# Optimization experiments

Measured on AMD Instinct MI355X. Metric: run time of the kernel, lower is better.

The kernel has to match this reference:

```python
import jax, jax.numpy as jnp
import numpy as np

INPUT_H = 512
INPUT_W = 512
POOL = 5
BN_EPS = 1e-5


def setup_inputs() -> dict:
    key = jax.random.key(0)
    ks = jax.random.split(key, 8)
    B = 16
    c3 = jax.random.normal(ks[0], (B, 512, 64, 64), jnp.float32)
    c4 = jax.random.normal(ks[1], (B, 1024, 32, 32), jnp.float32)
    xy = jax.random.uniform(ks[2], (B, 10, 4), jnp.float32) * 512.0
    # ensure x1<=x2, y1<=y2 like real detector boxes
    boxes = jnp.concatenate([jnp.minimum(xy[..., :2], xy[..., 2:]),
                             jnp.maximum(xy[..., :2], xy[..., 2:])], axis=-1)
    w_conv = jax.random.normal(ks[3], (512, 1536), jnp.float32) * 0.02  # 1x1 conv kernel
    b_conv = jnp.zeros((512,), jnp.float32)
    bn_gamma = jnp.ones((512,), jnp.float32)
    bn_beta = jnp.zeros((512,), jnp.float32)
    bn_mean = jax.random.normal(ks[4], (512,), jnp.float32) * 0.1
    bn_var = jax.random.uniform(ks[5], (512,), jnp.float32) * 0.5 + 0.5
    return {"c3": c3, "c4": c4, "boxes": boxes, "w_conv": w_conv, "b_conv": b_conv,
            "bn_gamma": bn_gamma, "bn_beta": bn_beta, "bn_mean": bn_mean, "bn_var": bn_var}


def _bin_weights(lo, hi, size, nout):
    """Adaptive-avg-pool bin weights over axis of length `size` for crop [lo,hi).
    Returns [nout, size] row-stochastic matrix (same math as AdaptiveAvgPool1d bins)."""
    length = hi - lo
    k = jnp.arange(nout)
    starts = lo + (k * length) // nout                      # floor(k*L/n)
    ends = lo + ((k + 1) * length + nout - 1) // nout        # ceil((k+1)*L/n)
    idx = jnp.arange(size)
    mask = (idx[None, :] >= starts[:, None]) & (idx[None, :] < ends[:, None])
    return mask.astype(jnp.float32) / (ends - starts)[:, None].astype(jnp.float32)


def reference(c3, c4, boxes, w_conv, b_conv, bn_gamma, bn_beta, bn_mean, bn_var):
    B = c3.shape[0]
    c4u = jax.image.resize(c4, (B, c4.shape[1], c4.shape[2] * 2, c4.shape[3] * 2),
                           method='bilinear')
    fused = jnp.concatenate([c3, c4u], axis=1)               # [B,1536,H,W]
    y = jnp.einsum('bchw,oc->bohw', fused, w_conv) + b_conv[None, :, None, None]
    inv = bn_gamma / jnp.sqrt(bn_var + BN_EPS)               # eval-mode BN
    y = y * inv[None, :, None, None] + (bn_beta - bn_mean * inv)[None, :, None, None]
    attr_blob = jax.nn.relu(y)                               # [B,512,H,W]
    H, W = attr_blob.shape[-2:]
    sx = W / INPUT_W
    sy = H / INPUT_H

    def pool_one(feat, box):  # feat [C,H,W], box [4] -> [C,5,5]
        x1 = jnp.clip(jnp.floor(box[0] * sx), 0, W - 1).astype(jnp.int32)
        y1 = jnp.clip(jnp.floor(box[1] * sy), 0, H - 1).astype(jnp.int32)
        x2 = jnp.clip(jnp.ceil(box[2] * sx), 0, W - 1).astype(jnp.int32)
        y2 = jnp.clip(jnp.ceil(box[3] * sy), 0, H - 1).astype(jnp.int32)
        x2 = jnp.where(x2 <= x1, jnp.minimum(x1 + 1, W), x2)
        y2 = jnp.where(y2 <= y1, jnp.minimum(y1 + 1, H), y2)
        wy = _bin_weights(y1, y2, H, POOL)                   # [5,H]
        wx = _bin_weights(x1, x2, W, POOL)                   # [5,W]
        return jnp.einsum('ph,chw,qw->cpq', wy, feat, wx)

    obj_blob = jax.vmap(lambda f, bx: jax.vmap(lambda b: pool_one(f, b))(bx))(attr_blob, boxes)
    return boxes, obj_blob  # ([B,10,4], [B,10,512,5,5])
```

## Files before the change

### kernel.cpp

```cpp
#include <hip/hip_runtime.h>
#include <stdint.h>

#define FH 64
#define FW 64
#define CIN 1536
#define C3C 512
#define C4C 1024
#define COUT 512
#define BATCH 16
#define NPIX 4096
#define NBOX 10
#define MPAD 256
#define NT 24

typedef float v4f __attribute__((ext_vector_type(4)));

#define GLOAD_LDS16(g, l) __builtin_amdgcn_global_load_lds( \
    (const __attribute__((address_space(1))) void*)(g),     \
    (__attribute__((address_space(3))) void*)(l), 16, 0, 0)

#define BARRIER() asm volatile("s_barrier" ::: "memory")

__device__ __forceinline__ uint32_t pack4_fp8(float a, float b, float c, float d) {
    int lo = __builtin_amdgcn_cvt_pk_fp8_f32(a, b, 0, false);
    int v  = __builtin_amdgcn_cvt_pk_fp8_f32(c, d, lo, true);
    return (uint32_t)v;
}
__device__ __forceinline__ unsigned char f32_to_fp8(float a) {
    return (unsigned char)(__builtin_amdgcn_cvt_pk_fp8_f32(a, a, 0, false) & 0xff);
}

__global__ void prep_bn(const float* __restrict__ bng, const float* __restrict__ bnb,
                        const float* __restrict__ bnm, const float* __restrict__ bnv,
                        const float* __restrict__ bconv,
                        float* __restrict__ scale, float* __restrict__ shift) {
    int o = threadIdx.x;
    if (o < COUT) {
        float inv = bng[o] / sqrtf(bnv[o] + 1e-5f);
        scale[o] = inv * 0.0625f;
        shift[o] = bnb[o] + inv * (bconv[o] - bnm[o]);
    }
}

__global__ void conv_w(const float* __restrict__ w, uint32_t* __restrict__ w8, int n4) {
    int i = blockIdx.x * 256 + threadIdx.x;
    if (i < n4) {
        float4 f = *(const float4*)(w + i * 4);
        w8[i] = pack4_fp8(f.x * 16.0f, f.y * 16.0f, f.z * 16.0f, f.w * 16.0f);
    }
}

__global__ __launch_bounds__(256) void build_fusedT(const float* __restrict__ c3,
                                                    const float* __restrict__ c4,
                                                    unsigned char* __restrict__ fusedT) {
    __shared__ uint32_t lds[64 * 36];
    int ct = blockIdx.x;
    int y  = blockIdx.y;
    int b  = blockIdx.z;
    int t  = threadIdx.x;
    int pg = t & 15;
    int cq = t >> 4;

    #pragma unroll
    for (int r = 0; r < 2; ++r) {
        int cquad = cq + 16 * r;
        float vv[4][4];
        if (ct < 4) {
            int ch = ct * 128 + 4 * cquad;
            const float* src = c3 + (((size_t)(b * C3C + ch) * FH + y) * FW) + 4 * pg;
            #pragma unroll
            for (int k = 0; k < 4; ++k) {
                float4 f = *(const float4*)(src + (size_t)k * (FH * FW));
                vv[k][0] = f.x; vv[k][1] = f.y; vv[k][2] = f.z; vv[k][3] = f.w;
            }
        } else {
            int ch = ct * 128 - 512 + 4 * cquad;
            int jy = y >> 1;
            int jyB = min(max(jy + ((y & 1) ? 1 : -1), 0), 31);
            const float* base = c4 + (size_t)(b * C4C + ch) * 1024;
            #pragma unroll
            for (int k = 0; k < 4; ++k) {
                const float* pc = base + (size_t)k * 1024;
                float2 f0 = *(const float2*)(pc + jy * 32 + 2 * pg);
                float2 f1 = *(const float2*)(pc + jyB * 32 + 2 * pg);
                float rbA = 0.75f * f0.x + 0.25f * f1.x;
                float rbB = 0.75f * f0.y + 0.25f * f1.y;
                float rbm = __shfl_up(rbB, 1, 16);
                float rbp = __shfl_down(rbA, 1, 16);
                if (pg == 0)  rbm = rbA;
                if (pg == 15) rbp = rbB;
                vv[k][0] = 0.75f * rbA + 0.25f * rbm;
                vv[k][1] = 0.75f * rbA + 0.25f * rbB;
                vv[k][2] = 0.75f * rbB + 0.25f * rbA;
                vv[k][3] = 0.75f * rbB + 0.25f * rbp;
            }
        }
        #pragma unroll
        for (int i = 0; i < 4; ++i) {
            int px = 4 * pg + i;
            lds[px * 36 + 4 * ((cquad >> 2) ^ ((px >> 1) & 7)) + (cquad & 3)] =
                pack4_fp8(vv[0][i], vv[1][i], vv[2][i], vv[3][i]);
        }
    }
    __syncthreads();
    int g = t & 7;
    #pragma unroll
    for (int rr = 0; rr < 2; ++rr) {
        int px = (t >> 3) + 32 * rr;
        uint4 w = *(const uint4*)(&lds[px * 36 + 4 * (g ^ ((px >> 1) & 7))]);
        *(uint4*)(fusedT + ((size_t)b * NPIX + y * FW + px) * CIN + ct * 128 + g * 16) = w;
    }
}

__global__ __launch_bounds__(512, 2) void gemm_bn_relu(
        const unsigned char* __restrict__ w8,
        const unsigned char* __restrict__ fusedT,
        const float* __restrict__ scale, const float* __restrict__ shift,
        unsigned char* __restrict__ attr) {
    __shared__ __align__(16) unsigned char lds_a[2][16384];
    __shared__ __align__(16) unsigned char lds_b[2][16384];
    const int t  = threadIdx.x;
    const int n0 = blockIdx.x * 256;
    const int o0 = blockIdx.y * 256;
    const int b  = blockIdx.z;
    const int wave = t >> 6, lane = t & 63;
    const int wm = wave & 1, wn = wave >> 1;
    const int quad = lane >> 4, l16 = lane & 15;
    const int q2 = quad >> 1, q1 = (quad & 1) * 8;
    const int keyq = (l16 >> 1) & 3;
    const int cs0 = ((q2 ^ keyq) * 16) + q1;
    const int cs1 = (((2 + q2) ^ keyq) * 16) + q1;
    const unsigned char* fb = fusedT + (size_t)b * NPIX * CIN;

    const int lrow = t >> 2;
    const int cg   = (t & 3) ^ ((t >> 3) & 3);
    const size_t gA0 = (size_t)(o0 + ((t >> 8) << 7) + (lrow & 63)) * CIN + cg * 16;
    const size_t gB0 = (size_t)(n0 + (((t >> 7) & 3) << 6) + (lrow & 31)) * CIN + cg * 16;

#define STAGE_A(tt, h, d) GLOAD_LDS16(w8 + gA0 + (size_t)(h) * (64 * CIN) + (size_t)(tt) * 64, \
                                      &lds_a[d][(h) * 8192 + t * 16])
#define STAGE_B(tt, h, d) GLOAD_LDS16(fb + gB0 + (size_t)(h) * (32 * CIN) + (size_t)(tt) * 64, \
                                      &lds_b[d][(h) * 8192 + t * 16])
#define RD_A(base, ih, i, csel) (*(const long*)((base) + (((ih) * 128 + wm * 64 + (i) * 16 + l16) << 6) + (csel)))
#define RD_B(base, jh, j, csel) (*(const long*)((base) + (((jh) * 128 + wn * 32 + (j) * 16 + l16) << 6) + (csel)))

    v4f acc[8][4];
    #pragma unroll
    for (int i = 0; i < 8; ++i)
        #pragma unroll
        for (int j = 0; j < 4; ++j) acc[i][j] = (v4f)0.0f;

    STAGE_A(0, 0, 0); STAGE_B(0, 0, 0);
    STAGE_A(0, 1, 0); STAGE_B(0, 1, 0);
    STAGE_A(1, 0, 1); STAGE_B(1, 0, 1);
    asm volatile("s_waitcnt vmcnt(2)" ::: "memory");
    BARRIER();

    long a0[4][2], a1[4][2], b0[2][2], b1[2][2];

    for (int kt = 0; kt < NT; ++kt) {
        const unsigned char* bA = lds_a[kt & 1];
        const unsigned char* bB = lds_b[kt & 1];
        const int cur = kt & 1, nxt = cur ^ 1;

        #pragma unroll
        for (int i = 0; i < 4; ++i) { a0[i][0] = RD_A(bA, 0, i, cs0); a0[i][1] = RD_A(bA, 0, i, cs1); }
        #pragma unroll
        for (int j = 0; j < 2; ++j) { b0[j][0] = RD_B(bB, 0, j, cs0); b0[j][1] = RD_B(bB, 0, j, cs1); }
        if (kt + 1 < NT) STAGE_A(kt + 1, 1, nxt);
        BARRIER();
        __builtin_amdgcn_s_setprio(1);
        #pragma unroll
        for (int s = 0; s < 2; ++s)
            #pragma unroll
            for (int i = 0; i < 4; ++i)
                #pragma unroll
                for (int j = 0; j < 2; ++j)
                    acc[i][j] = __builtin_amdgcn_mfma_f32_16x16x32_fp8_fp8(a0[i][s], b0[j][s], acc[i][j], 0, 0, 0);
        __builtin_amdgcn_s_setprio(0);
        BARRIER();

        #pragma unroll
        for (int j = 0; j < 2; ++j) { b1[j][0] = RD_B(bB, 1, j, cs0); b1[j][1] = RD_B(bB, 1, j, cs1); }
        if (kt + 1 < NT) STAGE_B(kt + 1, 1, nxt);
        BARRIER();
        __builtin_amdgcn_s_setprio(1);
        #pragma unroll
        for (int s = 0; s < 2; ++s)
            #pragma unroll
            for (int i = 0; i < 4; ++i)
                #pragma unroll
                for (int j = 0; j < 2; ++j)
                    acc[i][2 + j] = __builtin_amdgcn_mfma_f32_16x16x32_fp8_fp8(a0[i][s], b1[j][s], acc[i][2 + j], 0, 0, 0);
        __builtin_amdgcn_s_setprio(0);
        BARRIER();

        #pragma unroll
        for (int i = 0; i < 4; ++i) { a1[i][0] = RD_A(bA, 1, i, cs0); a1[i][1] = RD_A(bA, 1, i, cs1); }
        if (kt + 2 < NT) STAGE_A(kt + 2, 0, cur);
        BARRIER();
        __builtin_amdgcn_s_setprio(1);
        #pragma unroll
        for (int s = 0; s < 2; ++s)
            #pragma unroll
            for (int i = 0; i < 4; ++i)
                #pragma unroll
                for (int j = 0; j < 2; ++j)
                    acc[4 + i][j] = __builtin_amdgcn_mfma_f32_16x16x32_fp8_fp8(a1[i][s], b0[j][s], acc[4 + i][j], 0, 0, 0);
        __builtin_amdgcn_s_setprio(0);
        BARRIER();

        if (kt + 2 < NT) STAGE_B(kt + 2, 0, cur);
        BARRIER();
        __builtin_amdgcn_s_setprio(1);
        #pragma unroll
        for (int s = 0; s < 2; ++s)
            #pragma unroll
            for (int i = 0; i < 4; ++i)
                #pragma unroll
                for (int j = 0; j < 2; ++j)
                    acc[4 + i][2 + j] = __builtin_amdgcn_mfma_f32_16x16x32_fp8_fp8(a1[i][s], b1[j][s], acc[4 + i][2 + j], 0, 0, 0);
        __builtin_amdgcn_s_setprio(0);
        if (kt < NT - 2) { asm volatile("s_waitcnt vmcnt(2)" ::: "memory"); }
        else            { asm volatile("s_waitcnt vmcnt(0)" ::: "memory"); }
        BARRIER();
    }

    unsigned char* ab = attr + (size_t)b * COUT * NPIX;
    #pragma unroll
    for (int a = 0; a < 8; ++a) {
        int obase = o0 + wm * 128 + (a >> 2) * 64 + (a & 3) * 16 + quad * 4;
        #pragma unroll
        for (int r = 0; r < 4; ++r) {
            int oo = obase + r;
            float sc = scale[oo], sh = shift[oo];
            #pragma unroll
            for (int bb = 0; bb < 4; ++bb) {
                int n = n0 + wn * 64 + (bb >> 1) * 32 + (bb & 1) * 16 + l16;
                float v = fmaxf(acc[a][bb][r] * sc + sh, 0.0f);
                ab[(size_t)oo * NPIX + n] = f32_to_fp8(v);
            }
        }
    }
#undef STAGE_A
#undef STAGE_B
#undef RD_A
#undef RD_B
}

__global__ __launch_bounds__(256) void build_P(const float* __restrict__ boxes,
                                               unsigned char* __restrict__ P) {
    int br  = blockIdx.x;
    int m25 = blockIdx.y;
    int b   = br / NBOX;
    int m   = (br % NBOX) * 25 + m25;
    int p   = m25 / 5, q = m25 % 5;
    int t   = threadIdx.x;
    int y   = t >> 2;
    int x0  = (t & 3) * 16;
    const float* bx = boxes + (size_t)br * 4;
    int x1 = min(max((int)floorf(bx[0] * 0.125f), 0), 63);
    int y1 = min(max((int)floorf(bx[1] * 0.125f), 0), 63);
    int x2 = min(max((int)ceilf (bx[2] * 0.125f), 0), 63);
    int y2 = min(max((int)ceilf (bx[3] * 0.125f), 0), 63);
    if (x2 <= x1) x2 = min(x1 + 1, 64);
    if (y2 <= y1) y2 = min(y1 + 1, 64);
    int Lx = x2 - x1, Ly = y2 - y1;
    int sx = x1 + (q * Lx) / 5;
    int ex = x1 + ((q + 1) * Lx + 4) / 5;
    int sy = y1 + (p * Ly) / 5;
    int ey = y1 + ((p + 1) * Ly + 4) / 5;
    float wyv  = (y >= sy && y < ey) ? 1.0f / (float)(ey - sy) : 0.0f;
    float pval = 64.0f * wyv / (float)(ex - sx);
    float v[16];
    #pragma unroll
    for (int i = 0; i < 16; ++i) {
        int xi = x0 + i;
        v[i] = (xi >= sx && xi < ex) ? pval : 0.0f;
    }
    uint4 w;
    w.x = pack4_fp8(v[0],  v[1],  v[2],  v[3]);
    w.y = pack4_fp8(v[4],  v[5],  v[6],  v[7]);
    w.z = pack4_fp8(v[8],  v[9],  v[10], v[11]);
    w.w = pack4_fp8(v[12], v[13], v[14], v[15]);
    *(uint4*)(P + ((size_t)b * MPAD + m) * NPIX + y * FW + x0) = w;
}

__global__ __launch_bounds__(256) void pool_gemm(
        const unsigned char* __restrict__ P,
        const unsigned char* __restrict__ attr,
        float* __restrict__ part2) {
    __shared__ __align__(16) unsigned char lds_a[128 * 64];
    __shared__ __align__(16) unsigned char lds_b[128 * 64];
    int t  = threadIdx.x;
    int m0 = blockIdx.x * 128;
    int c0 = (blockIdx.y & 3) * 128;
    int seg = blockIdx.y >> 2;
    int b  = blockIdx.z;
    int wave = t >> 6, lane = t & 63;
    int wm = wave & 1, wn = wave >> 1;
    int quad = lane >> 4, l16 = lane & 15;
    const unsigned char* Pb = P + (size_t)b * MPAD * NPIX + seg * 1024;
    const unsigned char* ab = attr + (size_t)b * COUT * NPIX + seg * 1024;

    v4f acc[4][4];
    #pragma unroll
    for (int i = 0; i < 4; ++i)
        #pragma unroll
        for (int j = 0; j < 4; ++j) acc[i][j] = (v4f)0.0f;

    int row = t >> 2;
    int cg  = (t & 3) ^ ((row >> 1) & 3);
    const unsigned char* ga0 = Pb + (size_t)(m0 + row) * NPIX + cg * 16;
    const unsigned char* ga1 = Pb + (size_t)(m0 + row + 64) * NPIX + cg * 16;
    const unsigned char* gb0 = ab + (size_t)(c0 + row) * NPIX + cg * 16;
    const unsigned char* gb1 = ab + (size_t)(c0 + row + 64) * NPIX + cg * 16;
    unsigned char* la0 = lds_a + t * 16;
    unsigned char* la1 = lds_a + 4096 + t * 16;
    unsigned char* lb0 = lds_b + t * 16;
    unsigned char* lb1 = lds_b + 4096 + t * 16;

    int ra[4], rb[4];
    #pragma unroll
    for (int i = 0; i < 4; ++i) { ra[i] = wm * 64 + i * 16 + l16; rb[i] = wn * 64 + i * 16 + l16; }
    int q2 = quad >> 1, q1 = (quad & 1) * 8;

    for (int kt = 0; kt < 1024 / 64; ++kt) {
        __syncthreads();
        GLOAD_LDS16(ga0, la0);
        GLOAD_LDS16(ga1, la1);
        GLOAD_LDS16(gb0, lb0);
        GLOAD_LDS16(gb1, lb1);
        ga0 += 64; ga1 += 64; gb0 += 64; gb1 += 64;
        __syncthreads();

        #pragma unroll
        for (int s = 0; s < 2; ++s) {
            long af[4], bf[4];
            #pragma unroll
            for (int i = 0; i < 4; ++i) {
                int pa = (2 * s + q2) ^ ((ra[i] >> 1) & 3);
                af[i] = *(const long*)(lds_a + ra[i] * 64 + pa * 16 + q1);
                int pb = (2 * s + q2) ^ ((rb[i] >> 1) & 3);
                bf[i] = *(const long*)(lds_b + rb[i] * 64 + pb * 16 + q1);
            }
            #pragma unroll
            for (int i = 0; i < 4; ++i)
                #pragma unroll
                for (int j = 0; j < 4; ++j)
                    acc[i][j] = __builtin_amdgcn_mfma_f32_16x16x32_fp8_fp8(af[i], bf[j], acc[i][j], 0, 0, 0);
        }
    }

    float* pp = part2 + (((size_t)seg * BATCH + b) * MPAD) * COUT;
    #pragma unroll
    for (int i = 0; i < 4; ++i) {
        #pragma unroll
        for (int r = 0; r < 4; ++r) {
            int mrow = m0 + wm * 64 + i * 16 + quad * 4 + r;
            #pragma unroll
            for (int j = 0; j < 4; ++j) {
                int c = c0 + wn * 64 + j * 16 + l16;
                pp[(size_t)mrow * COUT + c] = acc[i][j][r];
            }
        }
    }
}

__global__ __launch_bounds__(256) void pool_reduce(const float* __restrict__ part2,
                                                   float* __restrict__ out) {
    const size_t SEG = (size_t)BATCH * MPAD * COUT;
    int i = blockIdx.x * 256 + threadIdx.x;
    int c = i & (COUT - 1);
    int m = (i >> 9) & (MPAD - 1);
    int b = i >> 17;
    if (m >= 250) return;
    float s = part2[i] + part2[i + SEG] + part2[i + 2 * SEG] + part2[i + 3 * SEG];
    int box = m / 25, bin = m - box * 25;
    out[640 + ((size_t)(b * NBOX + box) * COUT + c) * 25 + bin] = s * 0.015625f;
}

extern "C" void kernel_launch(void* const* d_in, const int* in_sizes, int n_in,
                              void* d_out, int out_size, void* d_ws, size_t ws_size,
                              hipStream_t stream) {
    const float* c3     = (const float*)d_in[0];
    const float* c4     = (const float*)d_in[1];
    const float* boxes  = (const float*)d_in[2];
    const float* w_conv = (const float*)d_in[3];
    const float* b_conv = (const float*)d_in[4];
    const float* bng    = (const float*)d_in[5];
    const float* bnb    = (const float*)d_in[6];
    const float* bnm    = (const float*)d_in[7];
    const float* bnv    = (const float*)d_in[8];
    float* out = (float*)d_out;

    char* ws = (char*)d_ws;
    unsigned char* fusedT = (unsigned char*)ws;
    unsigned char* P      = (unsigned char*)(ws + 100663296);
    float*         part2  = (float*)(ws + 117440512);
    unsigned char* w8     = (unsigned char*)(ws + 150994944);
    float*         scale  = (float*)(ws + 151781376);
    float*         shift  = (float*)(ws + 151783424);
    unsigned char* attr   = (unsigned char*)(ws + 151785472);

    hipMemcpyAsync(d_out, d_in[2], 640 * sizeof(float), hipMemcpyDeviceToDevice, stream);
    prep_bn<<<1, 512, 0, stream>>>(bng, bnb, bnm, bnv, b_conv, scale, shift);
    conv_w<<<(COUT * CIN / 4 + 255) / 256, 256, 0, stream>>>(w_conv, (uint32_t*)w8, COUT * CIN / 4);
    build_P<<<dim3(160, 25), 256, 0, stream>>>(boxes, P);
    build_fusedT<<<dim3(12, 64, 16), 256, 0, stream>>>(c3, c4, fusedT);
    gemm_bn_relu<<<dim3(16, 2, 16), 512, 0, stream>>>(w8, fusedT, scale, shift, attr);
    pool_gemm<<<dim3(2, 16, 16), 256, 0, stream>>>(P, attr, part2);
    pool_reduce<<<(BATCH * MPAD * COUT) / 256, 256, 0, stream>>>(part2, out);
    (void)in_sizes; (void)n_in; (void)out_size; (void)ws_size;
}
```

Measured before the change: 412.6 us.

## Deepen GEMM K-tile to 128 and restructure pipeline into two phases

The fp8 1x1-conv GEMM now stages 128-byte K slices per tile instead of 64, halving the number of K iterations and doubling LDS buffers to 64 KB each side. Each iteration runs two MFMA phases of 64 instructions with a new 8-way XOR swizzle, and load issue is split across the phases. This cuts barriers and loop overhead per K element and gives larger MFMA bursts, but raises LDS use to 128 KB per block, which may prevent two blocks per CU despite launch_bounds(512,2), and holds more fragments in registers.

Result: no change. 415.5 us (+0.7%).

```diff
diff --git a/kernel.cpp b/kernel.cpp
--- a/kernel.cpp
+++ b/kernel.cpp
@@ -11,7 +11,7 @@
 #define NPIX 4096
 #define NBOX 10
 #define MPAD 256
-#define NT 24
+#define KT128 12
 
 typedef float v4f __attribute__((ext_vector_type(4)));
 
@@ -117,8 +117,8 @@
         const unsigned char* __restrict__ fusedT,
         const float* __restrict__ scale, const float* __restrict__ shift,
         unsigned char* __restrict__ attr) {
-    __shared__ __align__(16) unsigned char lds_a[2][16384];
-    __shared__ __align__(16) unsigned char lds_b[2][16384];
+    __shared__ __align__(16) unsigned char lds_a[2][32768];
+    __shared__ __align__(16) unsigned char lds_b[2][32768];
     const int t  = threadIdx.x;
     const int n0 = blockIdx.x * 256;
     const int o0 = blockIdx.y * 256;
@@ -127,22 +127,22 @@
     const int wm = wave & 1, wn = wave >> 1;
     const int quad = lane >> 4, l16 = lane & 15;
     const int q2 = quad >> 1, q1 = (quad & 1) * 8;
-    const int keyq = (l16 >> 1) & 3;
-    const int cs0 = ((q2 ^ keyq) * 16) + q1;
-    const int cs1 = (((2 + q2) ^ keyq) * 16) + q1;
+    int cs[4];
+    #pragma unroll
+    for (int s = 0; s < 4; ++s) cs[s] = (((2 * s + q2) ^ (l16 & 7)) * 16) + q1;
     const unsigned char* fb = fusedT + (size_t)b * NPIX * CIN;
 
-    const int lrow = t >> 2;
-    const int cg   = (t & 3) ^ ((t >> 3) & 3);
-    const size_t gA0 = (size_t)(o0 + ((t >> 8) << 7) + (lrow & 63)) * CIN + cg * 16;
-    const size_t gB0 = (size_t)(n0 + (((t >> 7) & 3) << 6) + (lrow & 31)) * CIN + cg * 16;
-
-#define STAGE_A(tt, h, d) GLOAD_LDS16(w8 + gA0 + (size_t)(h) * (64 * CIN) + (size_t)(tt) * 64, \
-                                      &lds_a[d][(h) * 8192 + t * 16])
-#define STAGE_B(tt, h, d) GLOAD_LDS16(fb + gB0 + (size_t)(h) * (32 * CIN) + (size_t)(tt) * 64, \
-                                      &lds_b[d][(h) * 8192 + t * 16])
-#define RD_A(base, ih, i, csel) (*(const long*)((base) + (((ih) * 128 + wm * 64 + (i) * 16 + l16) << 6) + (csel)))
-#define RD_B(base, jh, j, csel) (*(const long*)((base) + (((jh) * 128 + wn * 32 + (j) * 16 + l16) << 6) + (csel)))
+    const int rr = t >> 3;
+    const int cg = (t & 7) ^ (rr & 7);
+    const unsigned char* gA = w8 + (size_t)(o0 + rr) * CIN + cg * 16;
+    const unsigned char* gB = fb + (size_t)(n0 + rr) * CIN + cg * 16;
+
+#define SA(u, kt, d) GLOAD_LDS16(gA + (size_t)(u) * (64 * CIN) + (kt) * 128, \
+                                 &lds_a[d][(u) * 8192 + t * 16])
+#define SB(u, kt, d) GLOAD_LDS16(gB + (size_t)(u) * (64 * CIN) + (kt) * 128, \
+                                 &lds_b[d][(u) * 8192 + t * 16])
+#define RA(d, ph, i, s) (*(const long*)(&lds_a[d][((wm * 128 + (ph) * 64 + (i) * 16 + l16) << 7) + cs[s]]))
+#define RB(d, j, s)     (*(const long*)(&lds_b[d][((wn * 64 + (j) * 16 + l16) << 7) + cs[s]]))
 
     v4f acc[8][4];
     #pragma unroll
@@ -150,79 +150,60 @@
         #pragma unroll
         for (int j = 0; j < 4; ++j) acc[i][j] = (v4f)0.0f;
 
-    STAGE_A(0, 0, 0); STAGE_B(0, 0, 0);
-    STAGE_A(0, 1, 0); STAGE_B(0, 1, 0);
-    STAGE_A(1, 0, 1); STAGE_B(1, 0, 1);
-    asm volatile("s_waitcnt vmcnt(2)" ::: "memory");
+    SA(0, 0, 0); SA(1, 0, 0); SA(2, 0, 0); SA(3, 0, 0);
+    SB(0, 0, 0); SB(1, 0, 0); SB(2, 0, 0); SB(3, 0, 0);
+    SA(0, 1, 1); SA(2, 1, 1); SB(0, 1, 1); SB(1, 1, 1); SB(2, 1, 1); SB(3, 1, 1);
+    asm volatile("s_waitcnt vmcnt(6)" ::: "memory");
     BARRIER();
 
-    long a0[4][2], a1[4][2], b0[2][2], b1[2][2];
-
-    for (int kt = 0; kt < NT; ++kt) {
-        const unsigned char* bA = lds_a[kt & 1];
-        const unsigned char* bB = lds_b[kt & 1];
+    long af[4][4], bf[4][4];
+
+    for (int kt = 0; kt < KT128; ++kt) {
         const int cur = kt & 1, nxt = cur ^ 1;
 
         #pragma unroll
-        for (int i = 0; i < 4; ++i) { a0[i][0] = RD_A(bA, 0, i, cs0); a0[i][1] = RD_A(bA, 0, i, cs1); }
-        #pragma unroll
-        for (int j = 0; j < 2; ++j) { b0[j][0] = RD_B(bB, 0, j, cs0); b0[j][1] = RD_B(bB, 0, j, cs1); }
-        if (kt + 1 < NT) STAGE_A(kt + 1, 1, nxt);
+        for (int i = 0; i < 4; ++i)
+            #pragma unroll
+            for (int s = 0; s < 4; ++s) af[i][s] = RA(cur, 0, i, s);
+        #pragma unroll
+        for (int j = 0; j < 4; ++j)
+            #pragma unroll
+            for (int s = 0; s < 4; ++s) bf[j][s] = RB(cur, j, s);
+        if (kt > 0 && kt + 1 < KT128) {
+            SA(0, kt + 1, nxt); SA(2, kt + 1, nxt);
+            SB(0, kt + 1, nxt); SB(1, kt + 1, nxt);
+            SB(2, kt + 1, nxt); SB(3, kt + 1, nxt);
+        }
         BARRIER();
         __builtin_amdgcn_s_setprio(1);
         #pragma unroll
-        for (int s = 0; s < 2; ++s)
+        for (int s = 0; s < 4; ++s)
             #pragma unroll
             for (int i = 0; i < 4; ++i)
                 #pragma unroll
-                for (int j = 0; j < 2; ++j)
-                    acc[i][j] = __builtin_amdgcn_mfma_f32_16x16x32_fp8_fp8(a0[i][s], b0[j][s], acc[i][j], 0, 0, 0);
+                for (int j = 0; j < 4; ++j)
+                    acc[i][j] = __builtin_amdgcn_mfma_f32_16x16x32_fp8_fp8(af[i][s], bf[j][s], acc[i][j], 0, 0, 0);
         __builtin_amdgcn_s_setprio(0);
+        if (kt + 1 < KT128) { asm volatile("s_waitcnt vmcnt(6)" ::: "memory"); }
+        else               { asm volatile("s_waitcnt vmcnt(0)" ::: "memory"); }
         BARRIER();
 
         #pragma unroll
-        for (int j = 0; j < 2; ++j) { b1[j][0] = RD_B(bB, 1, j, cs0); b1[j][1] = RD_B(bB, 1, j, cs1); }
-        if (kt + 1 < NT) STAGE_B(kt + 1, 1, nxt);
+        for (int i = 0; i < 4; ++i)
+            #pragma unroll
+            for (int s = 0; s < 4; ++s) af[i][s] = RA(cur, 1, i, s);
+        if (kt + 1 < KT128) { SA(1, kt + 1, nxt); SA(3, kt + 1, nxt); }
         BARRIER();
         __builtin_amdgcn_s_setprio(1);
         #pragma unroll
-        for (int s = 0; s < 2; ++s)
+        for (int s = 0; s < 4; ++s)
             #pragma unroll
             for (int i = 0; i < 4; ++i)
                 #pragma unroll
-                for (int j = 0; j < 2; ++j)
-                    acc[i][2 + j] = __builtin_amdgcn_mfma_f32_16x16x32_fp8_fp8(a0[i][s], b1[j][s], acc[i][2 + j], 0, 0, 0);
+                for (int j = 0; j < 4; ++j)
+                    acc[4 + i][j] = __builtin_amdgcn_mfma_f32_16x16x32_fp8_fp8(af[i][s], bf[j][s], acc[4 + i][j], 0, 0, 0);
         __builtin_amdgcn_s_setprio(0);
-        BARRIER();
-
-        #pragma unroll
-        for (int i = 0; i < 4; ++i) { a1[i][0] = RD_A(bA, 1, i, cs0); a1[i][1] = RD_A(bA, 1, i, cs1); }
-        if (kt + 2 < NT) STAGE_A(kt + 2, 0, cur);
-        BARRIER();
-        __builtin_amdgcn_s_setprio(1);
-        #pragma unroll
-        for (int s = 0; s < 2; ++s)
-            #pragma unroll
-            for (int i = 0; i < 4; ++i)
-                #pragma unroll
-                for (int j = 0; j < 2; ++j)
-                    acc[4 + i][j] = __builtin_amdgcn_mfma_f32_16x16x32_fp8_fp8(a1[i][s], b0[j][s], acc[4 + i][j], 0, 0, 0);
-        __builtin_amdgcn_s_setprio(0);
-        BARRIER();
-
-        if (kt + 2 < NT) STAGE_B(kt + 2, 0, cur);
-        BARRIER();
-        __builtin_amdgcn_s_setprio(1);
-        #pragma unroll
-        for (int s = 0; s < 2; ++s)
-            #pragma unroll
-            for (int i = 0; i < 4; ++i)
-                #pragma unroll
-                for (int j = 0; j < 2; ++j)
-                    acc[4 + i][2 + j] = __builtin_amdgcn_mfma_f32_16x16x32_fp8_fp8(a1[i][s], b1[j][s], acc[4 + i][2 + j], 0, 0, 0);
-        __builtin_amdgcn_s_setprio(0);
-        if (kt < NT - 2) { asm volatile("s_waitcnt vmcnt(2)" ::: "memory"); }
-        else            { asm volatile("s_waitcnt vmcnt(0)" ::: "memory"); }
+        if (kt + 1 < KT128) { asm volatile("s_waitcnt vmcnt(2)" ::: "memory"); }
         BARRIER();
     }
 
@@ -235,17 +216,17 @@
             int oo = obase + r;
             float sc = scale[oo], sh = shift[oo];
             #pragma unroll
-            for (int bb = 0; bb < 4; ++bb) {
-                int n = n0 + wn * 64 + (bb >> 1) * 32 + (bb & 1) * 16 + l16;
-                float v = fmaxf(acc[a][bb][r] * sc + sh, 0.0f);
+            for (int j = 0; j < 4; ++j) {
+                int n = n0 + wn * 64 + j * 16 + l16;
+                float v = fmaxf(acc[a][j][r] * sc + sh, 0.0f);
                 ab[(size_t)oo * NPIX + n] = f32_to_fp8(v);
             }
         }
     }
-#undef STAGE_A
-#undef STAGE_B
-#undef RD_A
-#undef RD_B
+#undef SA
+#undef SB
+#undef RA
+#undef RB
 }
 
 __global__ __launch_bounds__(256) void build_P(const float* __restrict__ boxes,
```
